# Performance work log

Hardware: AMD Instinct MI355X
Metric: run time of the kernel (lower is better)

Reference implementation:

```python
import jax, jax.numpy as jnp
import numpy as np

S = 3072        # total packed tokens
E = 1280        # d_model
H = 20          # encoder_attention_heads
D = E // H      # head_dim = 64
NSEG = 16       # number of packed audio chunks


def setup_inputs() -> dict:
    key = jax.random.key(0)
    ks = jax.random.split(key, 9)
    w = lambda k, shape: (jax.random.normal(k, shape, jnp.float32) * 0.02)
    hidden_states = jax.random.normal(ks[0], (S, E), jnp.float32)
    cu_seqlens = (jnp.arange(NSEG + 1, dtype=jnp.int32) * (S // NSEG))
    return {
        "hidden_states": hidden_states,
        "Wq": w(ks[1], (E, E)), "bq": w(ks[2], (E,)),
        "Wk": w(ks[3], (E, E)),                      # k_proj has no bias
        "Wv": w(ks[4], (E, E)), "bv": w(ks[5], (E,)),
        "Wo": w(ks[6], (E, E)), "bo": w(ks[7], (E,)),
        "cu_seqlens": cu_seqlens,
    }


def reference(hidden_states, Wq, bq, Wk, Wv, bv, Wo, bo, cu_seqlens):
    Sq, Em = hidden_states.shape
    Dh = Em // H
    # projections (torch Linear: x @ W.T + b)
    q = (hidden_states @ Wq.T + bq).reshape(Sq, H, Dh).transpose(1, 0, 2)  # [H,S,D]
    k = (hidden_states @ Wk.T).reshape(Sq, H, Dh).transpose(1, 0, 2)       # [H,S,D]
    v = (hidden_states @ Wv.T + bv).reshape(Sq, H, Dh).transpose(1, 0, 2)  # [H,S,D]
    # block-diagonal additive mask from cu_seqlens (vectorized equivalent of
    # the original Python loop): tokens attend only within their own segment.
    pos = jnp.arange(Sq)
    seg = jnp.searchsorted(cu_seqlens[1:], pos, side="right")              # segment id per token
    same = seg[:, None] == seg[None, :]                                    # [S,S]
    bias = jnp.where(same, 0.0, jnp.finfo(q.dtype).min)
    attn = jnp.einsum("hqd,hkd->hqk", q, k) / np.sqrt(Dh).astype(q.dtype)  # [H,S,S]
    attn = jax.nn.softmax(attn + bias, axis=-1)
    out = jnp.einsum("hqk,hkd->hqd", attn, v)                              # [H,S,D]
    out = out.transpose(1, 0, 2).reshape(Sq, Em)
    return out @ Wo.T + bo
```

## Files before the change

kernel.cpp:

```cpp
#include <hip/hip_runtime.h>
#include <hip/hip_bf16.h>
#include <stdint.h>

#define S_TOK 3072
#define E_DIM 1280
#define H_NUM 20
#define D_HEAD 64
#define NSEG 16

typedef __attribute__((ext_vector_type(8))) short short8;
typedef __attribute__((ext_vector_type(4))) float f32x4;

__device__ __forceinline__ unsigned short f2bf(float f){
  union { float f; unsigned int i; } u; u.f = f;
  unsigned int r = u.i + 0x7FFFu + ((u.i >> 16) & 1u);
  return (unsigned short)(r >> 16);
}

__device__ __forceinline__ void gload_lds16(const void* g, void* l){
  __builtin_amdgcn_global_load_lds((__attribute__((address_space(1))) void*)(g),
                                   (__attribute__((address_space(3))) void*)(l), 16, 0, 0);
}

__global__ void cvt_all(const float* __restrict__ hs,
                        const float* __restrict__ w0, const float* __restrict__ w1,
                        const float* __restrict__ w2,
                        unsigned short* __restrict__ hsb,
                        unsigned short* __restrict__ dqkv,
                        int nHS4, int nW4){
  int i = blockIdx.x * blockDim.x + threadIdx.x;
  const float* src;
  unsigned short* dst;
  size_t sj, dj;
  if (i < nHS4){
    src = hs; dst = hsb; sj = i; dj = i;
  } else {
    int t = i - nHS4;
    int w = t / nW4;
    if (w >= 3) return;
    int j = t - w * nW4;
    src = (w == 0) ? w0 : (w == 1) ? w1 : w2;
    sj = j;
    dst = dqkv; dj = (size_t)w * nW4 + j;
  }
  float4 v = reinterpret_cast<const float4*>(src)[sj];
  ushort4 o;
  o.x = f2bf(v.x); o.y = f2bf(v.y); o.z = f2bf(v.z); o.w = f2bf(v.w);
  reinterpret_cast<ushort4*>(dst)[dj] = o;
}

#define LGKM0 do { asm volatile("s_waitcnt lgkmcnt(0)" ::: "memory");         \
                   __builtin_amdgcn_sched_barrier(0); } while (0)
#define BAR   __builtin_amdgcn_s_barrier()

__global__ __launch_bounds__(512, 2) void gemm_qkv(
    const unsigned short* __restrict__ A,
    const unsigned short* __restrict__ Bp,
    const float* __restrict__ bias0,
    const float* __restrict__ bias1,
    unsigned short* __restrict__ Oq,
    unsigned short* __restrict__ Ok,
    unsigned short* __restrict__ Ov,
    int K)
{
  constexpr int SLOT = (192 + 256) * 64;
  __shared__ __align__(16) unsigned short SH[2 * SLOT];

  const int nwg = gridDim.x;
  const int xcd = blockIdx.x & 7, ix = blockIdx.x >> 3;
  const int wg = xcd * (nwg >> 3) + ix;
  const int st = wg / 20, ii = wg % 20;
  const int bm = (st / 3) * 4 + ii / 5;
  const int bn = (st % 3) * 5 + ii % 5;
  const int row0 = bm * 192, col0 = bn * 256;

  const int tid  = threadIdx.x;
  const int lane = tid & 63;
  const int w    = tid >> 6;
  const int wm   = w >> 2;
  const int wn   = w & 3;

  const f32x4 fz = {0.f, 0.f, 0.f, 0.f};
  f32x4 acc[4][3][2];
#pragma unroll
  for (int qd = 0; qd < 4; ++qd)
#pragma unroll
    for (int m = 0; m < 3; ++m)
#pragma unroll
      for (int n = 0; n < 2; ++n) acc[qd][m][n] = fz;

  auto stA = [&](int t){
    unsigned short* d = SH + (t & 1) * SLOT;
    const unsigned short* g = A + (size_t)row0 * K + (t << 6);
#pragma unroll
    for (int i = 0; i < 3; ++i){
      int s = i * 512 + tid;
      int r = s >> 3, ks = (s & 7) ^ (r & 7);
      gload_lds16(g + (size_t)r * K + ks * 8, d + s * 8);
    }
  };
  auto stB = [&](int h, int t){
    unsigned short* d = SH + (t & 1) * SLOT + 12288 + h * 8192;
    const unsigned short* g = Bp + (size_t)(col0 + h * 128) * K + (t << 6);
#pragma unroll
    for (int i = 0; i < 2; ++i){
      int s = i * 512 + tid;
      int r = s >> 3, ks = (s & 7) ^ (r & 7);
      gload_lds16(g + (size_t)r * K + ks * 8, d + s * 8);
    }
  };

  short8 af[3][2], bf0[2][2], bf1[2][2];
  auto RA = [&](int mh, int db){
    const unsigned short* Ah = SH + db * SLOT;
#pragma unroll
    for (int m = 0; m < 3; ++m){
      int ra = mh * 96 + wm * 48 + m * 16 + (lane & 15);
#pragma unroll
      for (int kk = 0; kk < 2; ++kk){
        int sl = kk * 4 + (lane >> 4);
        af[m][kk] = *reinterpret_cast<const short8*>(&Ah[ra * 64 + ((sl ^ (ra & 7))) * 8]);
      }
    }
  };
  auto RB = [&](int nh, int db, short8 (*bf)[2]){
    const unsigned short* Bb = SH + db * SLOT + 12288;
#pragma unroll
    for (int n = 0; n < 2; ++n){
      int rb = nh * 128 + wn * 32 + n * 16 + (lane & 15);
#pragma unroll
      for (int kk = 0; kk < 2; ++kk){
        int sl = kk * 4 + (lane >> 4);
        bf[n][kk] = *reinterpret_cast<const short8*>(&Bb[rb * 64 + ((sl ^ (rb & 7))) * 8]);
      }
    }
  };

#define MF_Q(QD, BF)                                                          \
  do {                                                                        \
    __builtin_amdgcn_s_setprio(1);                                            \
    _Pragma("unroll")                                                         \
    for (int kk = 0; kk < 2; ++kk)                                            \
      _Pragma("unroll")                                                       \
      for (int m = 0; m < 3; ++m)                                             \
        _Pragma("unroll")                                                     \
        for (int n = 0; n < 2; ++n)                                           \
          acc[QD][m][n] = __builtin_amdgcn_mfma_f32_16x16x32_bf16(            \
              af[m][kk], BF[n][kk], acc[QD][m][n], 0, 0, 0);                  \
    __builtin_amdgcn_s_setprio(0);                                            \
  } while (0)

  const int nk = K >> 6;
  stA(0); stB(0, 0); stB(1, 0);
  for (int t = 0; t < nk; ++t){
    const int db = t & 1;
    const bool nx = (t + 1 < nk);
    asm volatile("s_waitcnt vmcnt(2)" ::: "memory");
    BAR;
    RA(0, db); RB(0, db, bf0);
    if (nx) stA(t + 1);
    LGKM0; MF_Q(0, bf0);
    if (nx) asm volatile("s_waitcnt vmcnt(3)" ::: "memory");
    else    asm volatile("s_waitcnt vmcnt(0)" ::: "memory");
    BAR;
    RB(1, db, bf1);
    if (nx) stB(0, t + 1);
    LGKM0; MF_Q(1, bf1);
    BAR;
    RA(1, db);
    if (nx) stB(1, t + 1);
    LGKM0; MF_Q(2, bf1);
    BAR;
    MF_Q(3, bf0);
  }
  __syncthreads();

  {
    unsigned short* Cs = SH;
    const int CSTR = 264;
    const int mat = col0 / E_DIM;
    const int cc0 = col0 - mat * E_DIM;
    unsigned short* dst = (mat == 0) ? Oq : ((mat == 1) ? Ok : Ov);
    float bb[2][2];
#pragma unroll
    for (int nh = 0; nh < 2; ++nh)
#pragma unroll
      for (int n = 0; n < 2; ++n){
        int cc = cc0 + nh * 128 + wn * 32 + n * 16 + (lane & 15);
        bb[nh][n] = (mat == 0) ? bias0[cc] : (mat == 2 ? bias1[cc] : 0.0f);
      }
#pragma unroll
    for (int ph = 0; ph < 2; ++ph){
#pragma unroll
      for (int q2i = 0; q2i < 2; ++q2i){
        const int qd = ph * 2 + q2i;
        const int nh = (qd >> 1) ^ (qd & 1);
#pragma unroll
        for (int m = 0; m < 3; ++m)
#pragma unroll
          for (int n = 0; n < 2; ++n)
#pragma unroll
            for (int j = 0; j < 4; ++j){
              int rr = wm * 48 + m * 16 + (lane >> 4) * 4 + j;
              int c  = nh * 128 + wn * 32 + n * 16 + (lane & 15);
              Cs[rr * CSTR + c] = f2bf(acc[qd][m][n][j] + bb[nh][n]);
            }
      }
      __syncthreads();
#pragma unroll
      for (int i = 0; i < 6; ++i){
        int tk  = i * 512 + tid;
        int p   = tk / 768;
        int idx = tk - p * 768;
        int rr  = idx >> 3, sq = idx & 7;
        short8 vv = *reinterpret_cast<const short8*>(&Cs[rr * CSTR + p * 64 + sq * 8]);
        int gr = row0 + ph * 96 + rr;
        int hh = (cc0 >> 6) + p;
        *reinterpret_cast<short8*>(&dst[((size_t)hh * S_TOK + gr) * D_HEAD + sq * 8]) = vv;
      }
      __syncthreads();
    }
  }
#undef MF_Q
}

__global__ __launch_bounds__(256, 4) void gemm_out(
    const unsigned short* __restrict__ A,
    const unsigned short* __restrict__ Bp,
    const float* __restrict__ bias0,
    float* __restrict__ Of,
    int K)
{
  constexpr int SLOT = (64 + 128) * 32;
  __shared__ __align__(16) unsigned short SH[2 * SLOT];

  const int nwg = gridDim.x;
  const int xcd = blockIdx.x & 7, ix = blockIdx.x >> 3;
  const int wg = xcd * (nwg >> 3) + ix;
  const int bm = wg % 48;
  const int bn = wg / 48;
  const int row0 = bm * 64, col0 = bn * 128;

  const int tid  = threadIdx.x;
  const int lane = tid & 63;
  const int w    = tid >> 6;
  const int wm   = w >> 1;
  const int wn   = w & 1;

  const f32x4 fz = {0.f, 0.f, 0.f, 0.f};
  f32x4 acc[2][4];
#pragma unroll
  for (int m = 0; m < 2; ++m)
#pragma unroll
    for (int n = 0; n < 4; ++n) acc[m][n] = fz;

  auto stage = [&](int buf, int t){
    unsigned short* base = SH + buf * SLOT;
    const int k0 = t << 5;
#pragma unroll
    for (int i = 0; i < 3; ++i){
      int s = i * 256 + tid;
      int r = s >> 2, p = s & 3;
      int ks = p ^ ((r >> 1) & 3);
      const unsigned short* g = (r < 64)
          ? A  + (size_t)(row0 + r) * K + k0 + ks * 8
          : Bp + (size_t)(col0 + (r - 64)) * K + k0 + ks * 8;
      gload_lds16(g, base + s * 8);
    }
  };

  const int nk = K >> 5;
  stage(0, 0);
  int buf = 0;
  for (int t = 0; t < nk; ++t){
    asm volatile("s_waitcnt vmcnt(0)" ::: "memory");
    BAR;
    if (t + 1 < nk) stage(buf ^ 1, t + 1);
    const unsigned short* As = SH + buf * SLOT;
    const unsigned short* Bs = As + 64 * 32;
    short8 af[2], bf[4];
#pragma unroll
    for (int m = 0; m < 2; ++m){
      int ra = wm * 32 + m * 16 + (lane & 15);
      int sl = lane >> 4;
      af[m] = *reinterpret_cast<const short8*>(&As[ra * 32 + ((sl ^ ((ra >> 1) & 3))) * 8]);
    }
#pragma unroll
    for (int n = 0; n < 4; ++n){
      int rb = wn * 64 + n * 16 + (lane & 15);
      int sl = lane >> 4;
      bf[n] = *reinterpret_cast<const short8*>(&Bs[rb * 32 + ((sl ^ ((rb >> 1) & 3))) * 8]);
    }
    __builtin_amdgcn_s_setprio(1);
#pragma unroll
    for (int m = 0; m < 2; ++m)
#pragma unroll
      for (int n = 0; n < 4; ++n)
        acc[m][n] = __builtin_amdgcn_mfma_f32_16x16x32_bf16(af[m], bf[n], acc[m][n], 0, 0, 0);
    __builtin_amdgcn_s_setprio(0);
    buf ^= 1;
  }

  float bc[4];
#pragma unroll
  for (int n = 0; n < 4; ++n)
    bc[n] = bias0[col0 + wn * 64 + n * 16 + (lane & 15)];
#pragma unroll
  for (int m = 0; m < 2; ++m)
#pragma unroll
    for (int n = 0; n < 4; ++n){
      int c = col0 + wn * 64 + n * 16 + (lane & 15);
#pragma unroll
      for (int j = 0; j < 4; ++j){
        int r = row0 + wm * 32 + m * 16 + (lane >> 4) * 4 + j;
        Of[(size_t)r * E_DIM + c] = acc[m][n][j] + bc[n];
      }
    }
}

#define VSTR 200
#define PSTR 72
#define ATTN_BLKS (H_NUM * NSEG * 3)
__global__ __launch_bounds__(256, 3) void attn_kernel(
    const unsigned short* __restrict__ Q,
    const unsigned short* __restrict__ Kb,
    const unsigned short* __restrict__ V,
    const int* __restrict__ cu,
    unsigned short* __restrict__ O,
    const float* __restrict__ Wo,
    unsigned short* __restrict__ wob,
    int nW4)
{
  __shared__ __align__(16) unsigned short Vt[64*VSTR];
  __shared__ __align__(16) unsigned short Pw[4][16][PSTR];

  const int bid  = blockIdx.x;
  if (bid >= ATTN_BLKS){
    int i = (bid - ATTN_BLKS) * 256 + threadIdx.x;
    if (i < nW4){
      float4 v = reinterpret_cast<const float4*>(Wo)[i];
      ushort4 o;
      o.x = f2bf(v.x); o.y = f2bf(v.y); o.z = f2bf(v.z); o.w = f2bf(v.w);
      reinterpret_cast<ushort4*>(wob)[i] = o;
    }
    return;
  }
  const int unit = bid / 3;
  const int third= bid - unit*3;
  const int h    = unit >> 4;
  const int seg  = unit & 15;
  const int s0   = cu[seg];
  const int L    = cu[seg + 1] - s0;
  if (L <= 0) return;

  const int tid  = threadIdx.x;
  const int lane = tid & 63;
  const int w    = tid >> 6;
  const int row0g = third*64 + w*16;

  const unsigned short* qh = Q  + (size_t)h * S_TOK * D_HEAD;
  const unsigned short* kh = Kb + (size_t)h * S_TOK * D_HEAD;
  const unsigned short* vh = V  + (size_t)h * S_TOK * D_HEAD;

#pragma unroll
  for (int i = 0; i < 6; ++i){
    int task = i*256 + tid;
    int sr   = task % 192;
    int grp  = task / 192;
    int svr  = s0 + (sr < L ? sr : L - 1);
    short8 vv = *reinterpret_cast<const short8*>(vh + (size_t)svr*64 + grp*8);
#pragma unroll
    for (int j = 0; j < 8; ++j) Vt[(grp*8 + j)*VSTR + sr] = (unsigned short)vv[j];
  }

  short8 qf[2];
#pragma unroll
  for (int kk = 0; kk < 2; ++kk){
    int r  = row0g + (lane & 15);
    int sr = s0 + (r < L ? r : L - 1);
    qf[kk] = *reinterpret_cast<const short8*>(qh + (size_t)sr*64 + kk*32 + (lane >> 4)*8);
  }

  __syncthreads();

  const f32x4 fz = {0.f, 0.f, 0.f, 0.f};
  const float SCL = 0.125f * 1.44269504088896f;

  f32x4 sacc[12];
#pragma unroll
  for (int nt = 0; nt < 12; ++nt) sacc[nt] = fz;

#pragma unroll
  for (int nt = 0; nt < 12; ++nt){
    int rb = nt*16 + (lane & 15);
    int sr = s0 + (rb < L ? rb : L - 1);
    const unsigned short* kr = kh + (size_t)sr*64 + (lane >> 4)*8;
    short8 kf0 = *reinterpret_cast<const short8*>(kr);
    short8 kf1 = *reinterpret_cast<const short8*>(kr + 32);
    sacc[nt] = __builtin_amdgcn_mfma_f32_16x16x32_bf16(qf[0], kf0, sacc[nt], 0, 0, 0);
    sacc[nt] = __builtin_amdgcn_mfma_f32_16x16x32_bf16(qf[1], kf1, sacc[nt], 0, 0, 0);
  }

  float rinv[4];
#pragma unroll
  for (int j = 0; j < 4; ++j){
    float mx = -1e30f;
#pragma unroll
    for (int nt = 0; nt < 12; ++nt){
      int c = nt*16 + (lane & 15);
      float vv = (c < L) ? sacc[nt][j] : -1e30f;
      sacc[nt][j] = vv;
      mx = fmaxf(mx, vv);
    }
    mx = fmaxf(mx, __shfl_xor(mx, 1, 64));
    mx = fmaxf(mx, __shfl_xor(mx, 2, 64));
    mx = fmaxf(mx, __shfl_xor(mx, 4, 64));
    mx = fmaxf(mx, __shfl_xor(mx, 8, 64));
    float sum = 0.f;
#pragma unroll
    for (int nt = 0; nt < 12; ++nt){
      float pp = exp2f((sacc[nt][j] - mx) * SCL);
      sacc[nt][j] = pp;
      sum += pp;
    }
    sum += __shfl_xor(sum, 1, 64);
    sum += __shfl_xor(sum, 2, 64);
    sum += __shfl_xor(sum, 4, 64);
    sum += __shfl_xor(sum, 8, 64);
    rinv[j] = 1.0f / sum;
  }

  f32x4 oacc[4];
#pragma unroll
  for (int nt = 0; nt < 4; ++nt) oacc[nt] = fz;

#pragma unroll
  for (int kk = 0; kk < 6; ++kk){
#pragma unroll
    for (int ntl = 0; ntl < 2; ++ntl){
      int nt = kk*2 + ntl;
#pragma unroll
      for (int j = 0; j < 4; ++j)
        Pw[w][(lane >> 4)*4 + j][ntl*16 + (lane & 15)] = f2bf(sacc[nt][j]);
    }
    short8 pf = *reinterpret_cast<const short8*>(&Pw[w][lane & 15][(lane >> 4)*8]);
#pragma unroll
    for (int nt4 = 0; nt4 < 4; ++nt4){
      int dcol = nt4*16 + (lane & 15);
      short8 vf = *reinterpret_cast<const short8*>(&Vt[dcol*VSTR + kk*32 + (lane >> 4)*8]);
      oacc[nt4] = __builtin_amdgcn_mfma_f32_16x16x32_bf16(pf, vf, oacc[nt4], 0, 0, 0);
    }
  }

#pragma unroll
  for (int nt4 = 0; nt4 < 4; ++nt4)
#pragma unroll
    for (int j = 0; j < 4; ++j)
      Pw[w][(lane >> 4)*4 + j][nt4*16 + (lane & 15)] = f2bf(oacc[nt4][j] * rinv[j]);

  {
    int r = lane >> 2;
    int gr = row0g + r;
    if (gr < L){
#pragma unroll
      for (int part = 0; part < 2; ++part){
        int c0 = (lane & 3)*16 + part*8;
        short8 vv = *reinterpret_cast<const short8*>(&Pw[w][r][c0]);
        *reinterpret_cast<short8*>(&O[(size_t)(s0 + gr) * E_DIM + h*64 + c0]) = vv;
      }
    }
  }
}

extern "C" void kernel_launch(void* const* d_in, const int* in_sizes, int n_in,
                              void* d_out, int out_size, void* d_ws, size_t ws_size,
                              hipStream_t stream)
{
  const float* hs = (const float*)d_in[0];
  const float* Wq = (const float*)d_in[1];
  const float* bq = (const float*)d_in[2];
  const float* Wk = (const float*)d_in[3];
  const float* Wv = (const float*)d_in[4];
  const float* bv = (const float*)d_in[5];
  const float* Wo = (const float*)d_in[6];
  const float* bo = (const float*)d_in[7];
  const int*   cu = (const int*)d_in[8];
  float* out = (float*)d_out;

  unsigned short* p = (unsigned short*)d_ws;
  unsigned short* hsb  = p; p += (size_t)S_TOK * E_DIM;
  unsigned short* wqkv = p; p += (size_t)3 * E_DIM * E_DIM;
  unsigned short* wob  = p; p += (size_t)E_DIM * E_DIM;
  unsigned short* qb   = p; p += (size_t)S_TOK * E_DIM;
  unsigned short* kb   = p; p += (size_t)S_TOK * E_DIM;
  unsigned short* vb   = p; p += (size_t)S_TOK * E_DIM;
  unsigned short* aob  = p; p += (size_t)S_TOK * E_DIM;

  const int nHS4 = S_TOK * E_DIM / 4;
  const int nW4  = E_DIM * E_DIM / 4;
  const int nCvt = nHS4 + 3 * nW4;
  cvt_all<<<(nCvt + 255) / 256, 256, 0, stream>>>(hs, Wq, Wk, Wv, hsb, wqkv, nHS4, nW4);

  gemm_qkv<<<(S_TOK/192) * (3*E_DIM/256), 512, 0, stream>>>(
      hsb, wqkv, bq, bv, qb, kb, vb, E_DIM);

  const int cvtWoBlks = (nW4 + 255) / 256;
  attn_kernel<<<ATTN_BLKS + cvtWoBlks, 256, 0, stream>>>(
      qb, kb, vb, cu, aob, Wo, wob, nW4);

  gemm_out<<<(S_TOK/64) * (E_DIM/128), 256, 0, stream>>>(
      aob, wob, bo, out, E_DIM);
}
```

Baseline: 90.83 us.

## Enlarge output-projection GEMM tiles and add triple-buffered prefetch with grouped block mapping

Reworks the output-projection GEMM from 64x128 tiles with K-step 32 and 256 threads to 128x128 tiles with K-step 64 and 512 threads. It uses a three-slot LDS ring that issues the next stage before waiting, so loads overlap compute, and remaps workgroups into 4x5 groups for L2 reuse. The aim is more reuse per tile and fewer barriers per K. In exchange the grid shrinks from 480 to 240 blocks, which may underfill the GPU's compute units, and LDS use per block rises.

```diff
diff --git a/kernel.cpp b/kernel.cpp
--- a/kernel.cpp
+++ b/kernel.cpp
@@ -224,95 +224,105 @@
 #undef MF_Q
 }
 
-__global__ __launch_bounds__(256, 4) void gemm_out(
+__global__ __launch_bounds__(512, 2) void gemm_out(
     const unsigned short* __restrict__ A,
     const unsigned short* __restrict__ Bp,
     const float* __restrict__ bias0,
     float* __restrict__ Of,
     int K)
 {
-  constexpr int SLOT = (64 + 128) * 32;
-  __shared__ __align__(16) unsigned short SH[2 * SLOT];
+  constexpr int SLOT = 256 * 64;
+  __shared__ __align__(16) unsigned short SH[3 * SLOT];
 
   const int nwg = gridDim.x;
   const int xcd = blockIdx.x & 7, ix = blockIdx.x >> 3;
   const int wg = xcd * (nwg >> 3) + ix;
-  const int bm = wg % 48;
-  const int bn = wg / 48;
-  const int row0 = bm * 64, col0 = bn * 128;
+  const int st = wg / 20, ii = wg % 20;
+  const int bm = (st / 2) * 4 + ii / 5;
+  const int bn = (st % 2) * 5 + ii % 5;
+  const int row0 = bm * 128, col0 = bn * 128;
 
   const int tid  = threadIdx.x;
   const int lane = tid & 63;
   const int w    = tid >> 6;
-  const int wm   = w >> 1;
-  const int wn   = w & 1;
+  const int wm   = w >> 2;
+  const int wn   = w & 3;
 
   const f32x4 fz = {0.f, 0.f, 0.f, 0.f};
-  f32x4 acc[2][4];
-#pragma unroll
-  for (int m = 0; m < 2; ++m)
-#pragma unroll
-    for (int n = 0; n < 4; ++n) acc[m][n] = fz;
-
-  auto stage = [&](int buf, int t){
-    unsigned short* base = SH + buf * SLOT;
-    const int k0 = t << 5;
-#pragma unroll
-    for (int i = 0; i < 3; ++i){
-      int s = i * 256 + tid;
-      int r = s >> 2, p = s & 3;
-      int ks = p ^ ((r >> 1) & 3);
-      const unsigned short* g = (r < 64)
+  f32x4 acc[4][2];
+#pragma unroll
+  for (int m = 0; m < 4; ++m)
+#pragma unroll
+    for (int n = 0; n < 2; ++n) acc[m][n] = fz;
+
+  auto stage = [&](int sl, int t){
+    unsigned short* base = SH + sl * SLOT;
+    const int k0 = t << 6;
+#pragma unroll
+    for (int i = 0; i < 4; ++i){
+      int s = i * 512 + tid;
+      int r = s >> 3, ks = (s & 7) ^ (r & 7);
+      const unsigned short* g = (r < 128)
           ? A  + (size_t)(row0 + r) * K + k0 + ks * 8
-          : Bp + (size_t)(col0 + (r - 64)) * K + k0 + ks * 8;
+          : Bp + (size_t)(col0 + (r - 128)) * K + k0 + ks * 8;
       gload_lds16(g, base + s * 8);
     }
   };
 
-  const int nk = K >> 5;
+  const int nk = K >> 6;
   stage(0, 0);
-  int buf = 0;
   for (int t = 0; t < nk; ++t){
-    asm volatile("s_waitcnt vmcnt(0)" ::: "memory");
+    if (t + 1 < nk){
+      stage((t + 1) % 3, t + 1);
+      asm volatile("s_waitcnt vmcnt(4)" ::: "memory");
+    } else {
+      asm volatile("s_waitcnt vmcnt(0)" ::: "memory");
+    }
     BAR;
-    if (t + 1 < nk) stage(buf ^ 1, t + 1);
-    const unsigned short* As = SH + buf * SLOT;
-    const unsigned short* Bs = As + 64 * 32;
-    short8 af[2], bf[4];
-#pragma unroll
-    for (int m = 0; m < 2; ++m){
-      int ra = wm * 32 + m * 16 + (lane & 15);
-      int sl = lane >> 4;
-      af[m] = *reinterpret_cast<const short8*>(&As[ra * 32 + ((sl ^ ((ra >> 1) & 3))) * 8]);
-    }
-#pragma unroll
-    for (int n = 0; n < 4; ++n){
-      int rb = wn * 64 + n * 16 + (lane & 15);
-      int sl = lane >> 4;
-      bf[n] = *reinterpret_cast<const short8*>(&Bs[rb * 32 + ((sl ^ ((rb >> 1) & 3))) * 8]);
+    const unsigned short* As = SH + (t % 3) * SLOT;
+    const unsigned short* Bs = As + 128 * 64;
+    short8 af[4][2], bf[2][2];
+#pragma unroll
+    for (int m = 0; m < 4; ++m){
+      int ra = wm * 64 + m * 16 + (lane & 15);
+#pragma unroll
+      for (int kk = 0; kk < 2; ++kk){
+        int sl = kk * 4 + (lane >> 4);
+        af[m][kk] = *reinterpret_cast<const short8*>(&As[ra * 64 + ((sl ^ (ra & 7))) * 8]);
+      }
+    }
+#pragma unroll
+    for (int n = 0; n < 2; ++n){
+      int rb = wn * 32 + n * 16 + (lane & 15);
+#pragma unroll
+      for (int kk = 0; kk < 2; ++kk){
+        int sl = kk * 4 + (lane >> 4);
+        bf[n][kk] = *reinterpret_cast<const short8*>(&Bs[rb * 64 + ((sl ^ (rb & 7))) * 8]);
+      }
     }
     __builtin_amdgcn_s_setprio(1);
 #pragma unroll
-    for (int m = 0; m < 2; ++m)
-#pragma unroll
-      for (int n = 0; n < 4; ++n)
-        acc[m][n] = __builtin_amdgcn_mfma_f32_16x16x32_bf16(af[m], bf[n], acc[m][n], 0, 0, 0);
+    for (int kk = 0; kk < 2; ++kk)
+#pragma unroll
+      for (int m = 0; m < 4; ++m)
+#pragma unroll
+        for (int n = 0; n < 2; ++n)
+          acc[m][n] = __builtin_amdgcn_mfma_f32_16x16x32_bf16(af[m][kk], bf[n][kk], acc[m][n], 0, 0, 0);
     __builtin_amdgcn_s_setprio(0);
-    buf ^= 1;
-  }
-
-  float bc[4];
-#pragma unroll
-  for (int n = 0; n < 4; ++n)
-    bc[n] = bias0[col0 + wn * 64 + n * 16 + (lane & 15)];
-#pragma unroll
-  for (int m = 0; m < 2; ++m)
-#pragma unroll
-    for (int n = 0; n < 4; ++n){
-      int c = col0 + wn * 64 + n * 16 + (lane & 15);
+  }
+
+  float bc[2];
+#pragma unroll
+  for (int n = 0; n < 2; ++n)
+    bc[n] = bias0[col0 + wn * 32 + n * 16 + (lane & 15)];
+#pragma unroll
+  for (int m = 0; m < 4; ++m)
+#pragma unroll
+    for (int n = 0; n < 2; ++n){
+      int c = col0 + wn * 32 + n * 16 + (lane & 15);
 #pragma unroll
       for (int j = 0; j < 4; ++j){
-        int r = row0 + wm * 32 + m * 16 + (lane >> 4) * 4 + j;
+        int r = row0 + wm * 64 + m * 16 + (lane >> 4) * 4 + j;
         Of[(size_t)r * E_DIM + c] = acc[m][n][j] + bc[n];
       }
     }
@@ -508,6 +518,6 @@
   attn_kernel<<<ATTN_BLKS + cvtWoBlks, 256, 0, stream>>>(
       qb, kb, vb, cu, aob, Wo, wob, nW4);
 
-  gemm_out<<<(S_TOK/64) * (E_DIM/128), 256, 0, stream>>>(
+  gemm_out<<<(S_TOK/128) * (E_DIM/128), 512, 0, stream>>>(
       aob, wob, bo, out, E_DIM);
 }
```

Result: faster. 83.77 us (-7.8%).
